# Optimization experiments

Hardware: AMD Instinct MI355X
Metric: run time of the kernel (lower is better)

Reference implementation:

```python
import jax, jax.numpy as jnp
import numpy as np

NUM_TOKENS = 32
PAD_TOKEN = 1
DEL_COST = 1.0
INF = 1e9
EPS = 1e-7


def setup_inputs() -> dict:
    key = jax.random.key(0)
    k1, k2 = jax.random.split(key)
    y_true = jax.random.randint(k1, (32, 512), 0, NUM_TOKENS)
    y_pred = jax.random.uniform(k2, (32, 1024, NUM_TOKENS), dtype=jnp.float32)
    return {"y_true": y_true, "y_pred": y_pred}


def _left_shift(seq, pad_token):
    # remove internal pad tokens, shift real tokens left (stable)
    L = seq.shape[1]
    ixs = jnp.arange(L)
    keys = jnp.where(seq != pad_token, ixs[None, :], L + ixs[None, :])
    order = jnp.sort(keys, axis=1) % L
    return jnp.take_along_axis(seq, order, axis=1)


def _alignment(subs, ins, seq_lens):
    # subs: [b, m, n] substitution costs; ins: [b, n] insertion costs
    b, m, n = subs.shape
    dt = subs.dtype

    # wavefrontify subs -> [m+n-1, m, b]: out[k, i, :] = subs[:, i, k-i] (0 if oob)
    ks = jnp.arange(m + n - 1)[:, None]
    ii = jnp.arange(m)[None, :]
    jj = ks - ii
    subs_t = jnp.transpose(subs, (1, 2, 0))  # [m, n, b]
    subs_wf = jnp.where((jj >= 0) & (jj < n)[..., None] if False else ((jj >= 0) & (jj < n))[..., None],
                        subs_t[ii, jnp.clip(jj, 0, n - 1)], jnp.zeros((), dt))

    # wavefrontify ins -> [m+n, m+1, b]: out[k, i, :] = ins[:, k-i] (0 if oob)
    ks2 = jnp.arange(m + n)[:, None]
    ii2 = jnp.arange(m + 1)[None, :]
    jj2 = ks2 - ii2
    ins_t = jnp.transpose(ins, (1, 0))  # [n, b]
    ins_wf = jnp.where(((jj2 >= 0) & (jj2 < n))[..., None],
                       ins_t[jnp.clip(jj2, 0, n - 1)], jnp.zeros((), dt))

    i_range = jnp.arange(m + 1)
    batch_idx = jnp.arange(b)
    k_end = seq_lens + n  # antidiagonal where each sequence's answer lives

    # k=0 wavefront: D[0][0]=0 ; k=1 wavefront: D[0][1]=ins[0], D[1][0]=del
    v_p2 = jnp.concatenate([jnp.zeros((1, b), dt), jnp.full((m - 1, b), INF, dt)], 0)
    v_p1 = jnp.concatenate([ins_wf[0][:1], jnp.full((1, b), DEL_COST, dt),
                            jnp.full((m - 1, b), INF, dt)], 0)
    v_opt = jnp.full((b,), INF, dt)

    def step(carry, xs):
        v_p2, v_p1, v_opt = carry
        k, sub_k, ins_k = xs
        o_m = v_p2 + sub_k            # match:  D[i][j] + subs -> row i+1
        o_i = v_p1 + ins_k            # insert: D[i][j-1] + ins[j-1]
        v_p2n = v_p1[:-1]
        o_d = v_p2n + DEL_COST        # delete: D[i-1][j] + del
        rest = jnp.minimum(jnp.minimum(o_m, o_i[1:]), o_d)
        v_p1n = jnp.concatenate([o_i[:1], rest], 0)
        mask = ((k - i_range) >= 0) & ((k - i_range) <= n)
        v_p1n = jnp.where(mask[:, None], v_p1n, jnp.full((), INF, dt))
        v_opt = jnp.where(k_end == k, v_p1n[seq_lens, batch_idx], v_opt)
        return (v_p2n, v_p1n, v_opt), None

    ks_seq = jnp.arange(2, m + n + 1)
    (_, _, v_opt), _ = jax.lax.scan(step, (v_p2, v_p1, v_opt),
                                    (ks_seq, subs_wf, ins_wf[1:]))
    return v_opt


def reference(y_true, y_pred):
    y_true_ls = _left_shift(y_true, PAD_TOKEN)
    seq_lens = jnp.sum((y_true_ls != PAD_TOKEN).astype(jnp.int32), axis=-1)
    y_oh = jax.nn.one_hot(y_true_ls, NUM_TOKENS, dtype=y_pred.dtype)
    y_p = y_pred / jnp.sum(y_pred, axis=-1, keepdims=True)
    logp = jnp.log(jnp.clip(y_p, EPS, 1.0 - EPS))  # [b, n, t]
    subs = -jnp.einsum('bmt,bnt->bmn', y_oh, logp)  # sparse xent cost matrix
    ins = -jnp.log(jnp.clip(y_p[..., PAD_TOKEN], EPS, 1.0 - EPS))  # [b, n]
    loss = _alignment(subs, ins, seq_lens)
    return loss.sum()  # reduction='sum'
```

## Files before the change

kernel.cpp:

```cpp
#include <hip/hip_runtime.h>

#define NTOK 32
#define PADT 1
#define MLEN 512
#define NLEN 1024
#define EPS_F 1e-7f
#define CCH  128
#define NC   8
#define NWAVE 4
#define BSTRIDE 256
#define NL_PAD 128


template <bool MASKED>
__device__ __forceinline__ void do_iter(
    const float*& q0c, const float*& q1c, const float*& qic, const float*& qbc,
    float (&C0)[8], float (&C1)[8], float (&CI)[8], float (&CB)[8],
    float (&N0)[8], float (&N1)[8], float (&NI)[8], float (&NB)[8],
    float& dcur0, float& dcur1, float& diag0,
    int& sb, const int lane, float* __restrict__ bw)
{
  float wreg[8];
#pragma unroll
  for (int k = 0; k < 8; ++k) {
    N0[k] = q0c[8 + k]; N1[k] = q1c[8 + k];
    NI[k] = qic[8 + k]; NB[k] = qbc[8 + k];
  }
#pragma unroll
  for (int k = 0; k < 8; ++k) {
    float up0 = __int_as_float(__builtin_amdgcn_update_dpp(
        __float_as_int(CB[k]), __float_as_int(dcur1), 0x138, 0xF, 0xF, false));
    float a0 = diag0 + C0[k];
    float b0 = up0 + 1.0f;
    float c0 = dcur0 + CI[k];
    float m0 = fminf(fminf(a0, b0), c0);
    float a1 = dcur0 + C1[k];
    float b1 = m0 + 1.0f;
    float c1 = dcur1 + CI[k];
    float m1 = fminf(fminf(a1, b1), c1);
    if (MASKED) {
      int rsk = sb + k - lane;
      bool upd = rsk < CCH;
      bool act = ((unsigned)rsk) < (unsigned)CCH;
      diag0 = upd ? up0 : diag0;
      dcur0 = act ? m0 : dcur0;
      dcur1 = act ? m1 : dcur1;
    } else {
      diag0 = up0; dcur0 = m0; dcur1 = m1;
    }
    wreg[k] = m1;
  }
  if (lane == 63) {
    int slot0 = sb - 63;
#pragma unroll
    for (int k = 0; k < 8; ++k) {
      int sl = slot0 + k;
      if (MASKED) sl = (sl < 0) ? 0 : sl;
      bw[sl] = wreg[k];
    }
  }
  q0c += 8; q1c += 8; qic += 8; qbc += 8; sb += 8;
}

__global__ __launch_bounds__(256, 1) void align_loss_kernel(
    const int* __restrict__ y_true, const float* __restrict__ y_pred,
    float* __restrict__ partial)
{
  extern __shared__ float smem[];
  float* P0s  = smem;
  float* bnd  = P0s + 1280;
  int*   tok  = (int*)(bnd + 5 * 2 * BSTRIDE);
  float* wtmp = (float*)(tok + MLEN);
  int*   wti  = (int*)wtmp;
  float* nl   = wtmp + 16;

  const int b = blockIdx.x;
  const int t = threadIdx.x;
  const int lane = t & 63;
  const int wv = t >> 6;

  tok[t] = 0; tok[t + 256] = 0;
  __syncthreads();
  int total = 0;
  for (int h = 0; h < 2; ++h) {
    int yt = y_true[b * MLEN + h * 256 + t];
    bool f = (yt != PADT);
    unsigned long long m = __ballot(f);
    int wp = __popcll(m & ((1ull << lane) - 1ull));
    if (lane == 0) wti[8 + wv] = __popcll(m);
    __syncthreads();
    int offs = total, ht = 0;
#pragma unroll
    for (int w2 = 0; w2 < NWAVE; ++w2) { int cnt = wti[8 + w2]; if (w2 < wv) offs += cnt; ht += cnt; }
    if (f) tok[offs + wp] = yt;
    total += ht;
    __syncthreads();
  }
  const int L = total;

  for (int r = t; r < NLEN; r += 256) {
    const float4* rp = (const float4*)(y_pred + ((size_t)b * NLEN + r) * NTOK);
    float4 q[8]; float s = 0.f;
#pragma unroll
    for (int u = 0; u < 8; ++u) { q[u] = rp[u]; s += q[u].x + q[u].y + q[u].z + q[u].w; }
    float inv = 1.0f / s;
#pragma unroll
    for (int u = 0; u < 8; ++u) {
      float pv[4] = {q[u].x, q[u].y, q[u].z, q[u].w};
#pragma unroll
      for (int c2 = 0; c2 < 4; ++c2) {
        float p = pv[c2] * inv;
        p = fminf(fmaxf(p, EPS_F), 1.0f - EPS_F);
        nl[(u * 4 + c2) * NLEN + r] = -__logf(p);
      }
    }
  }
  __syncthreads();

  {
    float4 iv = *(const float4*)(nl + PADT * NLEN + 4 * t);
    float p1 = iv.x, p2 = iv.x + iv.y, p3 = p2 + iv.z, s4 = p3 + iv.w;
    float x = s4;
#pragma unroll
    for (int d = 1; d < 64; d <<= 1) {
      float y = __shfl_up(x, d);
      if (lane >= d) x += y;
    }
    if (lane == 63) wtmp[wv] = x;
    __syncthreads();
    float pre = x - s4;
#pragma unroll
    for (int w2 = 0; w2 < NWAVE; ++w2) if (w2 < wv) pre += wtmp[w2];
    *(float4*)(P0s + 4 * t) = make_float4(pre + p1, pre + p2, pre + p3, pre + s4);
  }

  const int r0 = 2 * t + 1;
  const int tk0 = tok[2 * t];
  const int tk1 = tok[2 * t + 1];
  const float* sub0 = nl + tk0 * NLEN;
  const float* sub1 = nl + tk1 * NLEN;
  const float* insp = nl + PADT * NLEN;
  float dcur0 = (float)r0;
  float dcur1 = (float)(r0 + 1);
  float diag0 = (float)(r0 - 1);

  for (int p = 0; p < NC + NWAVE - 1; ++p) {
    __syncthreads();
    const int c = p - wv;
    if (c < 0 || c >= NC) continue;
    const int base = c * CCH;
    const float* q0c = sub0 + base - lane;
    const float* q1c = sub1 + base - lane;
    const float* qic = insp + base - lane;
    const float* qbc = (wv == 0) ? (P0s + base)
                                 : (bnd + (wv * 2 + (p & 1)) * BSTRIDE);
    float* bw = bnd + ((wv + 1) * 2 + ((p + 1) & 1)) * BSTRIDE;

    float A0[8], A1[8], AI[8], AB[8], B0[8], B1[8], BI[8], BB[8];
#pragma unroll
    for (int k = 0; k < 8; ++k) { A0[k] = q0c[k]; A1[k] = q1c[k]; AI[k] = qic[k]; AB[k] = qbc[k]; }
    int sb = 0;
    for (int it2 = 0; it2 < 4; ++it2) {
      do_iter<true>(q0c, q1c, qic, qbc, A0, A1, AI, AB, B0, B1, BI, BB, dcur0, dcur1, diag0, sb, lane, bw);
      do_iter<true>(q0c, q1c, qic, qbc, B0, B1, BI, BB, A0, A1, AI, AB, dcur0, dcur1, diag0, sb, lane, bw);
    }
    for (int it2 = 0; it2 < 4; ++it2) {
      do_iter<false>(q0c, q1c, qic, qbc, A0, A1, AI, AB, B0, B1, BI, BB, dcur0, dcur1, diag0, sb, lane, bw);
      do_iter<false>(q0c, q1c, qic, qbc, B0, B1, BI, BB, A0, A1, AI, AB, dcur0, dcur1, diag0, sb, lane, bw);
    }
    for (int it2 = 0; it2 < 4; ++it2) {
      do_iter<true>(q0c, q1c, qic, qbc, A0, A1, AI, AB, B0, B1, BI, BB, dcur0, dcur1, diag0, sb, lane, bw);
      do_iter<true>(q0c, q1c, qic, qbc, B0, B1, BI, BB, A0, A1, AI, AB, dcur0, dcur1, diag0, sb, lane, bw);
    }
  }

  if (r0 == L) partial[b] = dcur0;
  if (r0 + 1 == L) partial[b] = dcur1;
  if (L == 0 && t == 0) partial[b] = P0s[NLEN - 1];
}

__global__ void reduce_kernel(const float* __restrict__ partial, float* __restrict__ out) {
  if (threadIdx.x == 0) {
    float s = 0.f;
    for (int b2 = 0; b2 < 32; ++b2) s += partial[b2];
    out[0] = s;
  }
}

extern "C" void kernel_launch(void* const* d_in, const int* in_sizes, int n_in,
                              void* d_out, int out_size, void* d_ws, size_t ws_size,
                              hipStream_t stream) {
  const int*   y_true = (const int*)d_in[0];
  const float* y_pred = (const float*)d_in[1];
  float* out = (float*)d_out;
  float* partial = (float*)d_ws;

  const size_t lds_words = 1280 + 5 * 2 * BSTRIDE + MLEN  + 16
                         + (size_t)NTOK * NLEN + NL_PAD;
  const size_t lds_bytes = lds_words * sizeof(float);

  hipFuncSetAttribute((const void*)align_loss_kernel,
                      hipFuncAttributeMaxDynamicSharedMemorySize, (int)lds_bytes);

  hipLaunchKernelGGL(align_loss_kernel, dim3(32), dim3(256), lds_bytes, stream,
                     y_true, y_pred, partial);
  hipLaunchKernelGGL(reduce_kernel, dim3(1), dim3(64), 0, stream, partial, out);
}
```

Measured before the change: 95.57 us.

## Process two columns per wavefront step with float2 loads and wider chunks

Each lane now computes a 2x2 cell block per step: two rows and two adjacent columns, using float2 LDS loads. Chunk width doubles to 256 columns with 4 chunks, so the wave pipeline has fewer stages and fewer block-wide barriers. The boundary exchange between waves is written as float2 per step, and the LDS layout is rearranged with a larger boundary stride. This trades more registers and a longer dependent chain per step for fewer steps, fewer syncs and a shorter pipeline fill/drain.

```diff
diff --git a/kernel.cpp b/kernel.cpp
--- a/kernel.cpp
+++ b/kernel.cpp
@@ -5,61 +5,58 @@
 #define MLEN 512
 #define NLEN 1024
 #define EPS_F 1e-7f
-#define CCH  128
-#define NC   8
+#define CCH 256
+#define NC 4
 #define NWAVE 4
-#define BSTRIDE 256
-#define NL_PAD 128
-
+#define BSTRIDE 416
+
+#define OFF_BND   0
+#define OFF_P0    (OFF_BND + 4*2*BSTRIDE)
+#define OFF_TOK   (OFF_P0 + 1184)
+#define OFF_WTMP  (OFF_TOK + 512)
+#define OFF_NL    (OFF_WTMP + 16)
+#define LDS_FLOATS (OFF_NL + NTOK*NLEN + 160)
 
 template <bool MASKED>
-__device__ __forceinline__ void do_iter(
-    const float*& q0c, const float*& q1c, const float*& qic, const float*& qbc,
-    float (&C0)[8], float (&C1)[8], float (&CI)[8], float (&CB)[8],
-    float (&N0)[8], float (&N1)[8], float (&NI)[8], float (&NB)[8],
-    float& dcur0, float& dcur1, float& diag0,
-    int& sb, const int lane, float* __restrict__ bw)
+__device__ __forceinline__ void do_iter2(
+    const float2*& q0, const float2*& q1, const float2*& qi, const float2*& qb,
+    float2 (&C0)[8], float2 (&C1)[8], float2 (&CI)[8], float2 (&CB)[8],
+    float2 (&N0)[8], float2 (&N1)[8], float2 (&NI)[8], float2 (&NB)[8],
+    float& s0, float& s1, float& pA, float& dgA,
+    int& sb, const int lane, float2* __restrict__ bw2)
 {
-  float wreg[8];
 #pragma unroll
   for (int k = 0; k < 8; ++k) {
-    N0[k] = q0c[8 + k]; N1[k] = q1c[8 + k];
-    NI[k] = qic[8 + k]; NB[k] = qbc[8 + k];
+    N0[k] = q0[8 + k]; N1[k] = q1[8 + k];
+    NI[k] = qi[8 + k]; NB[k] = qb[8 + k];
   }
 #pragma unroll
   for (int k = 0; k < 8; ++k) {
-    float up0 = __int_as_float(__builtin_amdgcn_update_dpp(
-        __float_as_int(CB[k]), __float_as_int(dcur1), 0x138, 0xF, 0xF, false));
-    float a0 = diag0 + C0[k];
-    float b0 = up0 + 1.0f;
-    float c0 = dcur0 + CI[k];
-    float m0 = fminf(fminf(a0, b0), c0);
-    float a1 = dcur0 + C1[k];
-    float b1 = m0 + 1.0f;
-    float c1 = dcur1 + CI[k];
-    float m1 = fminf(fminf(a1, b1), c1);
+    float upA = __int_as_float(__builtin_amdgcn_update_dpp(
+        __float_as_int(CB[k].x), __float_as_int(pA), 0x138, 0xF, 0xF, false));
+    float upB = __int_as_float(__builtin_amdgcn_update_dpp(
+        __float_as_int(CB[k].y), __float_as_int(s1), 0x138, 0xF, 0xF, false));
+    float mA0 = fminf(fminf(dgA + C0[k].x, upA + 1.0f), s0 + CI[k].x);
+    float mB0 = fminf(fminf(upA + C0[k].y, upB + 1.0f), mA0 + CI[k].y);
+    float mA1 = fminf(fminf(s0  + C1[k].x, mA0 + 1.0f), s1 + CI[k].x);
+    float mB1 = fminf(fminf(mA0 + C1[k].y, mB0 + 1.0f), mA1 + CI[k].y);
+    if (lane == 63) {
+      int sl = sb + k - 63;
+      if (MASKED) sl = sl < 0 ? 0 : sl;
+      bw2[sl] = make_float2(mA1, mB1);
+    }
     if (MASKED) {
       int rsk = sb + k - lane;
-      bool upd = rsk < CCH;
-      bool act = ((unsigned)rsk) < (unsigned)CCH;
-      diag0 = upd ? up0 : diag0;
-      dcur0 = act ? m0 : dcur0;
-      dcur1 = act ? m1 : dcur1;
+      bool act = ((unsigned)rsk) < 128u;
+      dgA = (rsk < 128) ? upB : dgA;
+      s0 = act ? mB0 : s0;
+      pA = act ? mA1 : pA;
+      s1 = act ? mB1 : s1;
     } else {
-      diag0 = up0; dcur0 = m0; dcur1 = m1;
-    }
-    wreg[k] = m1;
-  }
-  if (lane == 63) {
-    int slot0 = sb - 63;
-#pragma unroll
-    for (int k = 0; k < 8; ++k) {
-      int sl = slot0 + k;
-      if (MASKED) sl = (sl < 0) ? 0 : sl;
-      bw[sl] = wreg[k];
-    }
-  }
-  q0c += 8; q1c += 8; qic += 8; qbc += 8; sb += 8;
+      dgA = upB; s0 = mB0; pA = mA1; s1 = mB1;
+    }
+  }
+  q0 += 8; q1 += 8; qi += 8; qb += 8; sb += 8;
 }
 
 __global__ __launch_bounds__(256, 1) void align_loss_kernel(
@@ -67,12 +64,12 @@
     float* __restrict__ partial)
 {
   extern __shared__ float smem[];
-  float* P0s  = smem;
-  float* bnd  = P0s + 1280;
-  int*   tok  = (int*)(bnd + 5 * 2 * BSTRIDE);
-  float* wtmp = (float*)(tok + MLEN);
-  int*   wti  = (int*)wtmp;
-  float* nl   = wtmp + 16;
+  float* bnd   = smem + OFF_BND;
+  float* P0arr = smem + OFF_P0;
+  int*   tok   = (int*)(smem + OFF_TOK);
+  float* wtmp  = smem + OFF_WTMP;
+  int*   wti   = (int*)wtmp;
+  float* nl    = smem + OFF_NL;
 
   const int b = blockIdx.x;
   const int t = threadIdx.x;
@@ -131,7 +128,7 @@
     float pre = x - s4;
 #pragma unroll
     for (int w2 = 0; w2 < NWAVE; ++w2) if (w2 < wv) pre += wtmp[w2];
-    *(float4*)(P0s + 4 * t) = make_float4(pre + p1, pre + p2, pre + p3, pre + s4);
+    *(float4*)(P0arr + 4 * t) = make_float4(pre + p1, pre + p2, pre + p3, pre + s4);
   }
 
   const int r0 = 2 * t + 1;
@@ -140,43 +137,44 @@
   const float* sub0 = nl + tk0 * NLEN;
   const float* sub1 = nl + tk1 * NLEN;
   const float* insp = nl + PADT * NLEN;
-  float dcur0 = (float)r0;
-  float dcur1 = (float)(r0 + 1);
-  float diag0 = (float)(r0 - 1);
+  float s0  = (float)r0;
+  float s1  = (float)(r0 + 1);
+  float dgA = (float)(r0 - 1);
+  float pA  = (float)(r0 + 1);
 
   for (int p = 0; p < NC + NWAVE - 1; ++p) {
     __syncthreads();
     const int c = p - wv;
     if (c < 0 || c >= NC) continue;
     const int base = c * CCH;
-    const float* q0c = sub0 + base - lane;
-    const float* q1c = sub1 + base - lane;
-    const float* qic = insp + base - lane;
-    const float* qbc = (wv == 0) ? (P0s + base)
-                                 : (bnd + (wv * 2 + (p & 1)) * BSTRIDE);
-    float* bw = bnd + ((wv + 1) * 2 + ((p + 1) & 1)) * BSTRIDE;
-
-    float A0[8], A1[8], AI[8], AB[8], B0[8], B1[8], BI[8], BB[8];
-#pragma unroll
-    for (int k = 0; k < 8; ++k) { A0[k] = q0c[k]; A1[k] = q1c[k]; AI[k] = qic[k]; AB[k] = qbc[k]; }
+    const float2* q0 = (const float2*)(sub0 + base) - lane;
+    const float2* q1 = (const float2*)(sub1 + base) - lane;
+    const float2* qi = (const float2*)(insp + base) - lane;
+    const float2* qb = (wv == 0) ? (const float2*)(P0arr + base)
+                                 : (const float2*)(bnd + ((wv - 1) * 2 + (p & 1)) * BSTRIDE);
+    float2* bw2 = (float2*)(bnd + (wv * 2 + ((p + 1) & 1)) * BSTRIDE);
+
+    float2 A0[8], A1[8], AI[8], AB[8], B0[8], B1[8], BI[8], BB[8];
+#pragma unroll
+    for (int k = 0; k < 8; ++k) { A0[k] = q0[k]; A1[k] = q1[k]; AI[k] = qi[k]; AB[k] = qb[k]; }
     int sb = 0;
     for (int it2 = 0; it2 < 4; ++it2) {
-      do_iter<true>(q0c, q1c, qic, qbc, A0, A1, AI, AB, B0, B1, BI, BB, dcur0, dcur1, diag0, sb, lane, bw);
-      do_iter<true>(q0c, q1c, qic, qbc, B0, B1, BI, BB, A0, A1, AI, AB, dcur0, dcur1, diag0, sb, lane, bw);
+      do_iter2<true>(q0, q1, qi, qb, A0, A1, AI, AB, B0, B1, BI, BB, s0, s1, pA, dgA, sb, lane, bw2);
+      do_iter2<true>(q0, q1, qi, qb, B0, B1, BI, BB, A0, A1, AI, AB, s0, s1, pA, dgA, sb, lane, bw2);
     }
     for (int it2 = 0; it2 < 4; ++it2) {
-      do_iter<false>(q0c, q1c, qic, qbc, A0, A1, AI, AB, B0, B1, BI, BB, dcur0, dcur1, diag0, sb, lane, bw);
-      do_iter<false>(q0c, q1c, qic, qbc, B0, B1, BI, BB, A0, A1, AI, AB, dcur0, dcur1, diag0, sb, lane, bw);
+      do_iter2<false>(q0, q1, qi, qb, A0, A1, AI, AB, B0, B1, BI, BB, s0, s1, pA, dgA, sb, lane, bw2);
+      do_iter2<false>(q0, q1, qi, qb, B0, B1, BI, BB, A0, A1, AI, AB, s0, s1, pA, dgA, sb, lane, bw2);
     }
     for (int it2 = 0; it2 < 4; ++it2) {
-      do_iter<true>(q0c, q1c, qic, qbc, A0, A1, AI, AB, B0, B1, BI, BB, dcur0, dcur1, diag0, sb, lane, bw);
-      do_iter<true>(q0c, q1c, qic, qbc, B0, B1, BI, BB, A0, A1, AI, AB, dcur0, dcur1, diag0, sb, lane, bw);
-    }
-  }
-
-  if (r0 == L) partial[b] = dcur0;
-  if (r0 + 1 == L) partial[b] = dcur1;
-  if (L == 0 && t == 0) partial[b] = P0s[NLEN - 1];
+      do_iter2<true>(q0, q1, qi, qb, A0, A1, AI, AB, B0, B1, BI, BB, s0, s1, pA, dgA, sb, lane, bw2);
+      do_iter2<true>(q0, q1, qi, qb, B0, B1, BI, BB, A0, A1, AI, AB, s0, s1, pA, dgA, sb, lane, bw2);
+    }
+  }
+
+  if (r0 == L) partial[b] = s0;
+  if (r0 + 1 == L) partial[b] = s1;
+  if (L == 0 && t == 0) partial[b] = P0arr[NLEN - 1];
 }
 
 __global__ void reduce_kernel(const float* __restrict__ partial, float* __restrict__ out) {
@@ -195,10 +193,7 @@
   float* out = (float*)d_out;
   float* partial = (float*)d_ws;
 
-  const size_t lds_words = 1280 + 5 * 2 * BSTRIDE + MLEN  + 16
-                         + (size_t)NTOK * NLEN + NL_PAD;
-  const size_t lds_bytes = lds_words * sizeof(float);
-
+  const size_t lds_bytes = (size_t)LDS_FLOATS * sizeof(float);
   hipFuncSetAttribute((const void*)align_loss_kernel,
                       hipFuncAttributeMaxDynamicSharedMemorySize, (int)lds_bytes);
 
```

Measured after the change: 101.8 us. +6.5%, slower.

## Pack two batch rows per block with bf16 log-probability table in LDS

Applied to the files above, without the earlier changes.

Stores the negative log-probability table in LDS as bf16 instead of fp32, which halves its footprint so two batch elements fit in one 512-thread block. The grid shrinks from 32 to 16 blocks, each running two independent 256-thread teams that share block-wide barriers. This trades per-element precision of the substitution and insertion costs for LDS capacity, and adds bf16 conversion work in the inner loop. The two teams are coupled by the shared __syncthreads, which may add stalls.

```diff
diff --git a/kernel.cpp b/kernel.cpp
--- a/kernel.cpp
+++ b/kernel.cpp
@@ -8,13 +8,29 @@
 #define CCH  128
 #define NC   8
 #define NWAVE 4
+#define NPHASE (NC + NWAVE - 1)
 #define BSTRIDE 256
-#define NL_PAD 128
-
+
+#define TOFF_P0   0
+#define TOFF_BND  1280
+#define TOFF_TOK  3328
+#define TOFF_WT   3840
+#define TOFF_NL   3856
+#define TEAMF     20240
+#define LDS_FLOATS (2 * TEAMF + 64)
+
+__device__ __forceinline__ float bf2f(ushort v) {
+  return __uint_as_float(((unsigned)v) << 16);
+}
+__device__ __forceinline__ ushort f2bf(float x) {
+  unsigned u = __float_as_uint(x);
+  unsigned r = u + 0x7FFFu + ((u >> 16) & 1u);
+  return (ushort)(r >> 16);
+}
 
 template <bool MASKED>
 __device__ __forceinline__ void do_iter(
-    const float*& q0c, const float*& q1c, const float*& qic, const float*& qbc,
+    const ushort*& q0c, const ushort*& q1c, const ushort*& qic, const float*& qbc,
     float (&C0)[8], float (&C1)[8], float (&CI)[8], float (&CB)[8],
     float (&N0)[8], float (&N1)[8], float (&NI)[8], float (&NB)[8],
     float& dcur0, float& dcur1, float& diag0,
@@ -23,8 +39,8 @@
   float wreg[8];
 #pragma unroll
   for (int k = 0; k < 8; ++k) {
-    N0[k] = q0c[8 + k]; N1[k] = q1c[8 + k];
-    NI[k] = qic[8 + k]; NB[k] = qbc[8 + k];
+    N0[k] = bf2f(q0c[8 + k]); N1[k] = bf2f(q1c[8 + k]);
+    NI[k] = bf2f(qic[8 + k]); NB[k] = qbc[8 + k];
   }
 #pragma unroll
   for (int k = 0; k < 8; ++k) {
@@ -40,9 +56,8 @@
     float m1 = fminf(fminf(a1, b1), c1);
     if (MASKED) {
       int rsk = sb + k - lane;
-      bool upd = rsk < CCH;
       bool act = ((unsigned)rsk) < (unsigned)CCH;
-      diag0 = upd ? up0 : diag0;
+      diag0 = (rsk < CCH) ? up0 : diag0;
       dcur0 = act ? m0 : dcur0;
       dcur1 = act ? m1 : dcur1;
     } else {
@@ -62,44 +77,49 @@
   q0c += 8; q1c += 8; qic += 8; qbc += 8; sb += 8;
 }
 
-__global__ __launch_bounds__(256, 1) void align_loss_kernel(
+__global__ __launch_bounds__(512, 1) void align_loss_kernel(
     const int* __restrict__ y_true, const float* __restrict__ y_pred,
     float* __restrict__ partial)
 {
   extern __shared__ float smem[];
-  float* P0s  = smem;
-  float* bnd  = P0s + 1280;
-  int*   tok  = (int*)(bnd + 5 * 2 * BSTRIDE);
-  float* wtmp = (float*)(tok + MLEN);
-  int*   wti  = (int*)wtmp;
-  float* nl   = wtmp + 16;
-
-  const int b = blockIdx.x;
   const int t = threadIdx.x;
   const int lane = t & 63;
-  const int wv = t >> 6;
-
-  tok[t] = 0; tok[t + 256] = 0;
+  const int team = t >> 8;
+  const int tt = t & 255;
+  const int tw = (t >> 6) & 3;
+
+  float* sT   = smem + team * TEAMF;
+  float* P0s  = sT + TOFF_P0;
+  float* bnd  = sT + TOFF_BND;
+  int*   tok  = (int*)(sT + TOFF_TOK);
+  float* wtmp = sT + TOFF_WT;
+  int*   wti  = (int*)wtmp;
+  ushort* nlu = (ushort*)(sT + TOFF_NL);
+
+  const int bb = blockIdx.x * 2 + team;
+
+  tok[tt] = 0; tok[tt + 256] = 0;
   __syncthreads();
+
   int total = 0;
   for (int h = 0; h < 2; ++h) {
-    int yt = y_true[b * MLEN + h * 256 + t];
+    int yt = y_true[bb * MLEN + h * 256 + tt];
     bool f = (yt != PADT);
     unsigned long long m = __ballot(f);
     int wp = __popcll(m & ((1ull << lane) - 1ull));
-    if (lane == 0) wti[8 + wv] = __popcll(m);
+    if (lane == 0) wti[8 + tw] = __popcll(m);
     __syncthreads();
     int offs = total, ht = 0;
 #pragma unroll
-    for (int w2 = 0; w2 < NWAVE; ++w2) { int cnt = wti[8 + w2]; if (w2 < wv) offs += cnt; ht += cnt; }
+    for (int w2 = 0; w2 < NWAVE; ++w2) { int cnt = wti[8 + w2]; if (w2 < tw) offs += cnt; ht += cnt; }
     if (f) tok[offs + wp] = yt;
     total += ht;
     __syncthreads();
   }
   const int L = total;
 
-  for (int r = t; r < NLEN; r += 256) {
-    const float4* rp = (const float4*)(y_pred + ((size_t)b * NLEN + r) * NTOK);
+  for (int r = tt; r < NLEN; r += 256) {
+    const float4* rp = (const float4*)(y_pred + ((size_t)bb * NLEN + r) * NTOK);
     float4 q[8]; float s = 0.f;
 #pragma unroll
     for (int u = 0; u < 8; ++u) { q[u] = rp[u]; s += q[u].x + q[u].y + q[u].z + q[u].w; }
@@ -111,54 +131,58 @@
       for (int c2 = 0; c2 < 4; ++c2) {
         float p = pv[c2] * inv;
         p = fminf(fmaxf(p, EPS_F), 1.0f - EPS_F);
-        nl[(u * 4 + c2) * NLEN + r] = -__logf(p);
+        nlu[(u * 4 + c2) * NLEN + r] = f2bf(-__logf(p));
       }
     }
   }
   __syncthreads();
 
   {
-    float4 iv = *(const float4*)(nl + PADT * NLEN + 4 * t);
-    float p1 = iv.x, p2 = iv.x + iv.y, p3 = p2 + iv.z, s4 = p3 + iv.w;
+    const ushort4 iv4 = *(const ushort4*)(nlu + PADT * NLEN + 4 * tt);
+    float i0 = bf2f(iv4.x), i1 = bf2f(iv4.y), i2 = bf2f(iv4.z), i3 = bf2f(iv4.w);
+    float p1 = i0, p2 = i0 + i1, p3 = p2 + i2, s4 = p3 + i3;
     float x = s4;
 #pragma unroll
     for (int d = 1; d < 64; d <<= 1) {
       float y = __shfl_up(x, d);
       if (lane >= d) x += y;
     }
-    if (lane == 63) wtmp[wv] = x;
+    if (lane == 63) wtmp[tw] = x;
     __syncthreads();
     float pre = x - s4;
 #pragma unroll
-    for (int w2 = 0; w2 < NWAVE; ++w2) if (w2 < wv) pre += wtmp[w2];
-    *(float4*)(P0s + 4 * t) = make_float4(pre + p1, pre + p2, pre + p3, pre + s4);
-  }
-
-  const int r0 = 2 * t + 1;
-  const int tk0 = tok[2 * t];
-  const int tk1 = tok[2 * t + 1];
-  const float* sub0 = nl + tk0 * NLEN;
-  const float* sub1 = nl + tk1 * NLEN;
-  const float* insp = nl + PADT * NLEN;
+    for (int w2 = 0; w2 < NWAVE; ++w2) if (w2 < tw) pre += wtmp[w2];
+    *(float4*)(P0s + 4 * tt) = make_float4(pre + p1, pre + p2, pre + p3, pre + s4);
+  }
+
+  const int r0 = 2 * tt + 1;
+  const int tk0 = tok[2 * tt];
+  const int tk1 = tok[2 * tt + 1];
+  const ushort* sub0 = nlu + tk0 * NLEN;
+  const ushort* sub1 = nlu + tk1 * NLEN;
+  const ushort* insp = nlu + PADT * NLEN;
   float dcur0 = (float)r0;
   float dcur1 = (float)(r0 + 1);
   float diag0 = (float)(r0 - 1);
 
-  for (int p = 0; p < NC + NWAVE - 1; ++p) {
-    __syncthreads();
-    const int c = p - wv;
+  for (int p = 0; p < NPHASE; ++p) {
+    __syncthreads();
+    const int c = p - tw;
     if (c < 0 || c >= NC) continue;
     const int base = c * CCH;
-    const float* q0c = sub0 + base - lane;
-    const float* q1c = sub1 + base - lane;
-    const float* qic = insp + base - lane;
-    const float* qbc = (wv == 0) ? (P0s + base)
-                                 : (bnd + (wv * 2 + (p & 1)) * BSTRIDE);
-    float* bw = bnd + ((wv + 1) * 2 + ((p + 1) & 1)) * BSTRIDE;
+    const ushort* q0c = sub0 + base - lane;
+    const ushort* q1c = sub1 + base - lane;
+    const ushort* qic = insp + base - lane;
+    const float* qbc = (tw == 0) ? (P0s + base)
+                                 : (bnd + ((tw - 1) * 2 + (p & 1)) * BSTRIDE);
+    float* bw = bnd + (tw * 2 + ((p + 1) & 1)) * BSTRIDE;
 
     float A0[8], A1[8], AI[8], AB[8], B0[8], B1[8], BI[8], BB[8];
 #pragma unroll
-    for (int k = 0; k < 8; ++k) { A0[k] = q0c[k]; A1[k] = q1c[k]; AI[k] = qic[k]; AB[k] = qbc[k]; }
+    for (int k = 0; k < 8; ++k) {
+      A0[k] = bf2f(q0c[k]); A1[k] = bf2f(q1c[k]);
+      AI[k] = bf2f(qic[k]); AB[k] = qbc[k];
+    }
     int sb = 0;
     for (int it2 = 0; it2 < 4; ++it2) {
       do_iter<true>(q0c, q1c, qic, qbc, A0, A1, AI, AB, B0, B1, BI, BB, dcur0, dcur1, diag0, sb, lane, bw);
@@ -174,9 +198,9 @@
     }
   }
 
-  if (r0 == L) partial[b] = dcur0;
-  if (r0 + 1 == L) partial[b] = dcur1;
-  if (L == 0 && t == 0) partial[b] = P0s[NLEN - 1];
+  if (r0 == L) partial[bb] = dcur0;
+  if (r0 + 1 == L) partial[bb] = dcur1;
+  if (L == 0 && tt == 0) partial[bb] = P0s[NLEN - 1];
 }
 
 __global__ void reduce_kernel(const float* __restrict__ partial, float* __restrict__ out) {
@@ -195,14 +219,11 @@
   float* out = (float*)d_out;
   float* partial = (float*)d_ws;
 
-  const size_t lds_words = 1280 + 5 * 2 * BSTRIDE + MLEN  + 16
-                         + (size_t)NTOK * NLEN + NL_PAD;
-  const size_t lds_bytes = lds_words * sizeof(float);
-
+  const size_t lds_bytes = (size_t)LDS_FLOATS * sizeof(float);
   hipFuncSetAttribute((const void*)align_loss_kernel,
                       hipFuncAttributeMaxDynamicSharedMemorySize, (int)lds_bytes);
 
-  hipLaunchKernelGGL(align_loss_kernel, dim3(32), dim3(256), lds_bytes, stream,
+  hipLaunchKernelGGL(align_loss_kernel, dim3(16), dim3(512), lds_bytes, stream,
                      y_true, y_pred, partial);
   hipLaunchKernelGGL(reduce_kernel, dim3(1), dim3(64), 0, stream, partial, out);
 }
```

Result: slower. 192.7 us (+101.6%).

## Store negative log-probs as bf16 with shifted copy, pack LDS loads

Applied to the files above, without the earlier changes.

The per-token cost table in LDS becomes bf16 and is stored twice, once as is and once shifted by one element, so each lane can fetch two costs per 32-bit load whatever its parity. The lane-63 boundary writes become float4 stores, and the boundary buffers are re-indexed to a tighter layout. This cuts LDS bytes loaded per anti-diagonal step in the wavefront DP. The price is bf16 rounding of every substitution and insertion cost, which can shift the summed loss beyond fp32 accuracy.

```diff
diff --git a/kernel.cpp b/kernel.cpp
--- a/kernel.cpp
+++ b/kernel.cpp
@@ -8,58 +8,76 @@
 #define CCH  128
 #define NC   8
 #define NWAVE 4
+#define NPHASE (NC + NWAVE - 1)
 #define BSTRIDE 256
-#define NL_PAD 128
-
+
+#define OFF_P0   0
+#define OFF_BND  1280
+#define OFF_TOK  3072
+#define OFF_WT   3584
+#define OFF_NLA  3600
+#define OFF_NLB  19984
+#define LDS_FLOATS (OFF_NLB + 16384 + 128)
+
+__device__ __forceinline__ float min3f(float a, float b, float c) {
+  return fminf(fminf(a, b), c);
+}
+__device__ __forceinline__ float dpp_shr1(float old_v, float src) {
+  return __int_as_float(__builtin_amdgcn_update_dpp(
+      __float_as_int(old_v), __float_as_int(src), 0x138, 0xF, 0xF, false));
+}
+__device__ __forceinline__ ushort f2bf(float x) {
+  unsigned u = __float_as_uint(x);
+  unsigned r = u + 0x7FFFu + ((u >> 16) & 1u);
+  return (ushort)(r >> 16);
+}
 
 template <bool MASKED>
 __device__ __forceinline__ void do_iter(
-    const float*& q0c, const float*& q1c, const float*& qic, const float*& qbc,
+    const unsigned*& tp0, const unsigned*& tp1, const unsigned*& tpi,
+    const float*& qbc,
     float (&C0)[8], float (&C1)[8], float (&CI)[8], float (&CB)[8],
     float (&N0)[8], float (&N1)[8], float (&NI)[8], float (&NB)[8],
     float& dcur0, float& dcur1, float& diag0,
-    int& sb, const int lane, float* __restrict__ bw)
+    int& sb, const int lane, float* __restrict__ bw,
+    float& wq0, float& wq1, float& wq2, float& wq3)
 {
-  float wreg[8];
+#pragma unroll
+  for (int m = 0; m < 4; ++m) {
+    unsigned u0 = tp0[4 + m];
+    unsigned u1 = tp1[4 + m];
+    unsigned ui = tpi[4 + m];
+    N0[2*m] = __uint_as_float(u0 << 16);  N0[2*m+1] = __uint_as_float(u0 & 0xFFFF0000u);
+    N1[2*m] = __uint_as_float(u1 << 16);  N1[2*m+1] = __uint_as_float(u1 & 0xFFFF0000u);
+    NI[2*m] = __uint_as_float(ui << 16);  NI[2*m+1] = __uint_as_float(ui & 0xFFFF0000u);
+    float2 vb = *(const float2*)(qbc + 8 + 2*m);
+    NB[2*m] = vb.x; NB[2*m+1] = vb.y;
+  }
 #pragma unroll
   for (int k = 0; k < 8; ++k) {
-    N0[k] = q0c[8 + k]; N1[k] = q1c[8 + k];
-    NI[k] = qic[8 + k]; NB[k] = qbc[8 + k];
-  }
-#pragma unroll
-  for (int k = 0; k < 8; ++k) {
-    float up0 = __int_as_float(__builtin_amdgcn_update_dpp(
-        __float_as_int(CB[k]), __float_as_int(dcur1), 0x138, 0xF, 0xF, false));
-    float a0 = diag0 + C0[k];
-    float b0 = up0 + 1.0f;
-    float c0 = dcur0 + CI[k];
-    float m0 = fminf(fminf(a0, b0), c0);
-    float a1 = dcur0 + C1[k];
-    float b1 = m0 + 1.0f;
-    float c1 = dcur1 + CI[k];
-    float m1 = fminf(fminf(a1, b1), c1);
+    float up0 = dpp_shr1(CB[k], dcur1);
+    float m0 = min3f(diag0 + C0[k], up0 + 1.0f, dcur0 + CI[k]);
+    float m1 = min3f(dcur0 + C1[k], m0 + 1.0f, dcur1 + CI[k]);
     if (MASKED) {
       int rsk = sb + k - lane;
-      bool upd = rsk < CCH;
       bool act = ((unsigned)rsk) < (unsigned)CCH;
-      diag0 = upd ? up0 : diag0;
+      diag0 = (rsk < CCH) ? up0 : diag0;
       dcur0 = act ? m0 : dcur0;
       dcur1 = act ? m1 : dcur1;
     } else {
       diag0 = up0; dcur0 = m0; dcur1 = m1;
     }
-    wreg[k] = m1;
-  }
-  if (lane == 63) {
-    int slot0 = sb - 63;
-#pragma unroll
-    for (int k = 0; k < 8; ++k) {
-      int sl = slot0 + k;
-      if (MASKED) sl = (sl < 0) ? 0 : sl;
-      bw[sl] = wreg[k];
-    }
-  }
-  q0c += 8; q1c += 8; qic += 8; qbc += 8; sb += 8;
+    switch ((k + 1) & 3) {
+      case 0: wq0 = m1; break; case 1: wq1 = m1; break;
+      case 2: wq2 = m1; break; case 3: wq3 = m1; break;
+    }
+    if (k == 2 || k == 6) {
+      int q63 = sb + k - 63;
+      if (lane == 63 && q63 >= 3 && q63 < 128)
+        *(float4*)(bw + (q63 - 3)) = make_float4(wq0, wq1, wq2, wq3);
+    }
+  }
+  tp0 += 4; tp1 += 4; tpi += 4; qbc += 8; sb += 8;
 }
 
 __global__ __launch_bounds__(256, 1) void align_loss_kernel(
@@ -67,12 +85,13 @@
     float* __restrict__ partial)
 {
   extern __shared__ float smem[];
-  float* P0s  = smem;
-  float* bnd  = P0s + 1280;
-  int*   tok  = (int*)(bnd + 5 * 2 * BSTRIDE);
-  float* wtmp = (float*)(tok + MLEN);
+  float* P0s  = smem + OFF_P0;
+  float* bnd  = smem + OFF_BND;
+  int*   tok  = (int*)(smem + OFF_TOK);
+  float* wtmp = smem + OFF_WT;
   int*   wti  = (int*)wtmp;
-  float* nl   = wtmp + 16;
+  ushort* nlA = (ushort*)(smem + OFF_NLA);
+  ushort* nlB = (ushort*)(smem + OFF_NLB);
 
   const int b = blockIdx.x;
   const int t = threadIdx.x;
@@ -81,6 +100,7 @@
 
   tok[t] = 0; tok[t + 256] = 0;
   __syncthreads();
+
   int total = 0;
   for (int h = 0; h < 2; ++h) {
     int yt = y_true[b * MLEN + h * 256 + t];
@@ -111,15 +131,22 @@
       for (int c2 = 0; c2 < 4; ++c2) {
         float p = pv[c2] * inv;
         p = fminf(fmaxf(p, EPS_F), 1.0f - EPS_F);
-        nl[(u * 4 + c2) * NLEN + r] = -__logf(p);
+        ushort v = f2bf(-__logf(p));
+        int tk = u * 4 + c2;
+        nlA[tk * 1024 + r] = v;
+        if (r > 0) nlB[tk * 1024 + r - 1] = v;
       }
     }
   }
   __syncthreads();
 
   {
-    float4 iv = *(const float4*)(nl + PADT * NLEN + 4 * t);
-    float p1 = iv.x, p2 = iv.x + iv.y, p3 = p2 + iv.z, s4 = p3 + iv.w;
+    const ushort4 iv4 = *(const ushort4*)(nlA + PADT * 1024 + 4 * t);
+    float i0v = __uint_as_float(((unsigned)iv4.x) << 16);
+    float i1v = __uint_as_float(((unsigned)iv4.y) << 16);
+    float i2v = __uint_as_float(((unsigned)iv4.z) << 16);
+    float i3v = __uint_as_float(((unsigned)iv4.w) << 16);
+    float p1 = i0v, p2 = i0v + i1v, p3 = p2 + i2v, s4 = p3 + i3v;
     float x = s4;
 #pragma unroll
     for (int d = 1; d < 64; d <<= 1) {
@@ -137,40 +164,53 @@
   const int r0 = 2 * t + 1;
   const int tk0 = tok[2 * t];
   const int tk1 = tok[2 * t + 1];
-  const float* sub0 = nl + tk0 * NLEN;
-  const float* sub1 = nl + tk1 * NLEN;
-  const float* insp = nl + PADT * NLEN;
   float dcur0 = (float)r0;
   float dcur1 = (float)(r0 + 1);
   float diag0 = (float)(r0 - 1);
-
-  for (int p = 0; p < NC + NWAVE - 1; ++p) {
+  float wq0 = 0, wq1 = 0, wq2 = 0, wq3 = 0;
+
+  const unsigned* baseA = (const unsigned*)nlA;
+  const unsigned* baseB = (const unsigned*)nlB;
+
+  for (int p = 0; p < NPHASE; ++p) {
     __syncthreads();
     const int c = p - wv;
     if (c < 0 || c >= NC) continue;
     const int base = c * CCH;
-    const float* q0c = sub0 + base - lane;
-    const float* q1c = sub1 + base - lane;
-    const float* qic = insp + base - lane;
+    const int i0 = base - lane;
+    const int par = i0 & 1;
+    const int joff = (i0 - par) >> 1;
+    const unsigned* tb = par ? baseB : baseA;
+    const unsigned* tp0 = tb + tk0 * 512 + joff;
+    const unsigned* tp1 = tb + tk1 * 512 + joff;
+    const unsigned* tpi = tb + PADT * 512 + joff;
     const float* qbc = (wv == 0) ? (P0s + base)
-                                 : (bnd + (wv * 2 + (p & 1)) * BSTRIDE);
-    float* bw = bnd + ((wv + 1) * 2 + ((p + 1) & 1)) * BSTRIDE;
+                                 : (bnd + ((wv - 1) * 2 + (p & 1)) * BSTRIDE);
+    float* bw = (wv < 3) ? (bnd + (wv * 2 + ((p + 1) & 1)) * BSTRIDE)
+                         : (bnd + 6 * BSTRIDE);
 
     float A0[8], A1[8], AI[8], AB[8], B0[8], B1[8], BI[8], BB[8];
 #pragma unroll
-    for (int k = 0; k < 8; ++k) { A0[k] = q0c[k]; A1[k] = q1c[k]; AI[k] = qic[k]; AB[k] = qbc[k]; }
+    for (int m = 0; m < 4; ++m) {
+      unsigned u0 = tp0[m], u1 = tp1[m], ui = tpi[m];
+      A0[2*m] = __uint_as_float(u0 << 16); A0[2*m+1] = __uint_as_float(u0 & 0xFFFF0000u);
+      A1[2*m] = __uint_as_float(u1 << 16); A1[2*m+1] = __uint_as_float(u1 & 0xFFFF0000u);
+      AI[2*m] = __uint_as_float(ui << 16); AI[2*m+1] = __uint_as_float(ui & 0xFFFF0000u);
+      float2 vb = *(const float2*)(qbc + 2*m);
+      AB[2*m] = vb.x; AB[2*m+1] = vb.y;
+    }
     int sb = 0;
     for (int it2 = 0; it2 < 4; ++it2) {
-      do_iter<true>(q0c, q1c, qic, qbc, A0, A1, AI, AB, B0, B1, BI, BB, dcur0, dcur1, diag0, sb, lane, bw);
-      do_iter<true>(q0c, q1c, qic, qbc, B0, B1, BI, BB, A0, A1, AI, AB, dcur0, dcur1, diag0, sb, lane, bw);
+      do_iter<true>(tp0, tp1, tpi, qbc, A0, A1, AI, AB, B0, B1, BI, BB, dcur0, dcur1, diag0, sb, lane, bw, wq0, wq1, wq2, wq3);
+      do_iter<true>(tp0, tp1, tpi, qbc, B0, B1, BI, BB, A0, A1, AI, AB, dcur0, dcur1, diag0, sb, lane, bw, wq0, wq1, wq2, wq3);
     }
     for (int it2 = 0; it2 < 4; ++it2) {
-      do_iter<false>(q0c, q1c, qic, qbc, A0, A1, AI, AB, B0, B1, BI, BB, dcur0, dcur1, diag0, sb, lane, bw);
-      do_iter<false>(q0c, q1c, qic, qbc, B0, B1, BI, BB, A0, A1, AI, AB, dcur0, dcur1, diag0, sb, lane, bw);
+      do_iter<false>(tp0, tp1, tpi, qbc, A0, A1, AI, AB, B0, B1, BI, BB, dcur0, dcur1, diag0, sb, lane, bw, wq0, wq1, wq2, wq3);
+      do_iter<false>(tp0, tp1, tpi, qbc, B0, B1, BI, BB, A0, A1, AI, AB, dcur0, dcur1, diag0, sb, lane, bw, wq0, wq1, wq2, wq3);
     }
     for (int it2 = 0; it2 < 4; ++it2) {
-      do_iter<true>(q0c, q1c, qic, qbc, A0, A1, AI, AB, B0, B1, BI, BB, dcur0, dcur1, diag0, sb, lane, bw);
-      do_iter<true>(q0c, q1c, qic, qbc, B0, B1, BI, BB, A0, A1, AI, AB, dcur0, dcur1, diag0, sb, lane, bw);
+      do_iter<true>(tp0, tp1, tpi, qbc, A0, A1, AI, AB, B0, B1, BI, BB, dcur0, dcur1, diag0, sb, lane, bw, wq0, wq1, wq2, wq3);
+      do_iter<true>(tp0, tp1, tpi, qbc, B0, B1, BI, BB, A0, A1, AI, AB, dcur0, dcur1, diag0, sb, lane, bw, wq0, wq1, wq2, wq3);
     }
   }
 
@@ -195,10 +235,7 @@
   float* out = (float*)d_out;
   float* partial = (float*)d_ws;
 
-  const size_t lds_words = 1280 + 5 * 2 * BSTRIDE + MLEN  + 16
-                         + (size_t)NTOK * NLEN + NL_PAD;
-  const size_t lds_bytes = lds_words * sizeof(float);
-
+  const size_t lds_bytes = (size_t)LDS_FLOATS * sizeof(float);
   hipFuncSetAttribute((const void*)align_loss_kernel,
                       hipFuncAttributeMaxDynamicSharedMemorySize, (int)lds_bytes);
 
```

Measured after the change: 95.94 us. Within noise of the previous version (+0.4%).
